# Kernel tuning notes

Measured on AMD Instinct MI355X. Metric: run time of the kernel, lower is better.

## Reference

```python
import jax, jax.numpy as jnp
import numpy as np

B, S, D, H = 2, 2048, 512, 8
HD = D // H
EPS = 1e-5


def _ln(x, g, b):
    mu = jnp.mean(x, axis=-1, keepdims=True)
    var = jnp.mean((x - mu) ** 2, axis=-1, keepdims=True)
    return (x - mu) * jax.lax.rsqrt(var + EPS) * g + b


def setup_inputs() -> dict:
    key = jax.random.key(0)
    ks = jax.random.split(key, 16)
    x = jax.random.normal(ks[0], (B, S, D), dtype=jnp.float32)
    adj = jax.random.randint(ks[1], (B, S, S), 0, 2, dtype=jnp.int32)
    adj = adj.at[:, jnp.arange(S), jnp.arange(S)].set(1)  # self-loops, avoid all-masked rows
    edge_attr = jax.random.normal(ks[2], (B, S, S), dtype=jnp.float32)
    sc = 1.0 / np.sqrt(D)
    p = lambda k, shp: jax.random.normal(k, shp, dtype=jnp.float32) * sc
    return {
        "x": x, "adj_matrix": adj, "edge_attr_matrix": edge_attr,
        "ln1_g": jnp.ones((D,)), "ln1_b": jnp.zeros((D,)),
        "ln2_g": jnp.ones((D,)), "ln2_b": jnp.zeros((D,)),
        "wq": p(ks[3], (D, D)), "bq": jnp.zeros((D,)),
        "wk": p(ks[4], (D, D)), "bk": jnp.zeros((D,)),
        "wv": p(ks[5], (D, D)), "bv": jnp.zeros((D,)),
        "wo": p(ks[6], (D, D)), "bo": jnp.zeros((D,)),
        "w1": p(ks[7], (D, 4 * D)), "b1": jnp.zeros((4 * D,)),
        "w2": p(ks[8], (4 * D, D)), "b2": jnp.zeros((D,)),
    }


def reference(x, adj_matrix, edge_attr_matrix, ln1_g, ln1_b, ln2_g, ln2_b,
              wq, bq, wk, bk, wv, bv, wo, bo, w1, b1, w2, b2):
    b, s, d = x.shape
    residual = x
    nx = _ln(x, ln1_g, ln1_b)
    q = (nx @ wq + bq).reshape(b, s, H, HD).transpose(0, 2, 1, 3)  # [B,H,S,HD]
    k = (nx @ wk + bk).reshape(b, s, H, HD).transpose(0, 2, 1, 3)
    v = (nx @ wv + bv).reshape(b, s, H, HD).transpose(0, 2, 1, 3)
    adjf = adj_matrix.astype(jnp.float32)
    # bias: -inf where no edge, else 0.1*edge_attr*adj (faithful to score_mod)
    bias = jnp.where(adj_matrix > 0, 0.1 * edge_attr_matrix * adjf, -jnp.inf)[:, None]  # [B,1,S,S]
    scores = jnp.einsum('bhqd,bhkd->bhqk', q, k) / np.sqrt(HD) + bias
    attn = jax.nn.softmax(scores, axis=-1)
    out = jnp.einsum('bhqk,bhkd->bhqd', attn, v)
    out = out.transpose(0, 2, 1, 3).reshape(b, s, d)
    x1 = residual + (out @ wo + bo)
    n2 = _ln(x1, ln2_g, ln2_b)
    mlp = jax.nn.gelu(n2 @ w1 + b1, approximate=False) @ w2 + b2
    return x1 + mlp
```

## Files before the change

kernel.cpp:

```cpp
#include <hip/hip_runtime.h>
#include <cstdint>
#include <cstddef>

typedef __bf16 bf16x8 __attribute__((ext_vector_type(8)));
typedef float f32x4 __attribute__((ext_vector_type(4)));
typedef const __attribute__((address_space(1))) void* gas_t;
typedef __attribute__((address_space(3))) void* las_t;

#define QSCALE 0.18033688011112042f
#define BSCALE 0.14426950408889634f

__device__ __forceinline__ unsigned short f2bf(float f) {
  union { float f; unsigned u; } v; v.f = f;
  unsigned r = v.u + 0x7FFFu + ((v.u >> 16) & 1u);
  return (unsigned short)(r >> 16);
}
__device__ __forceinline__ float bf2f(unsigned short h) {
  union { unsigned u; float f; } v; v.u = ((unsigned)h) << 16;
  return v.f;
}
__device__ __forceinline__ unsigned pack_bf16(float p0, float p1) {
  union { float f; unsigned u; } a, b; a.f = p0; b.f = p1;
  return __builtin_amdgcn_perm(b.u + 0x8000u, a.u + 0x8000u, 0x07060302u);
}
__device__ __forceinline__ void gll16(const void* g, void* l) {
  __builtin_amdgcn_global_load_lds((gas_t)g, (las_t)l, 16, 0, 0);
}

struct TPAll { const float* in[6]; unsigned short* out[6]; int R[6]; int C[6]; };
__global__ __launch_bounds__(256) void transpose_all(TPAll p) {
  const int z = blockIdx.z;
  int bxb = blockIdx.x, byb = blockIdx.y;
  if (z == 5) { int t = bxb; bxb = byb; byb = t; }
  const int R = p.R[z], C = p.C[z];
  const int bx = bxb * 32, by = byb * 32;
  if (bx >= C || by >= R) return;
  const float* in = p.in[z];
  unsigned short* out = p.out[z];
  __shared__ float tile[32][33];
  int tx = threadIdx.x & 31, tg = threadIdx.x >> 5;
  #pragma unroll
  for (int i = 0; i < 4; i++) {
    int r = tg * 4 + i;
    tile[r][tx] = in[(size_t)(by + r) * C + bx + tx];
  }
  __syncthreads();
  #pragma unroll
  for (int i = 0; i < 4; i++) {
    int r = tg * 4 + i;
    out[(size_t)(bx + r) * R + by + tx] = f2bf(tile[tx][r]);
  }
}

__global__ __launch_bounds__(256) void bias_pack(const int* __restrict__ adj,
                                                 const float* __restrict__ edge,
                                                 unsigned short* __restrict__ bp) {
  size_t i = ((size_t)blockIdx.x * 256 + threadIdx.x) * 4;
  int4 a = *(const int4*)(adj + i);
  float4 e = *(const float4*)(edge + i);
  ushort4 r;
  r.x = a.x > 0 ? f2bf(BSCALE * e.x * (float)a.x - 20.0f) : f2bf(-30000.0f);
  r.y = a.y > 0 ? f2bf(BSCALE * e.y * (float)a.y - 20.0f) : f2bf(-30000.0f);
  r.z = a.z > 0 ? f2bf(BSCALE * e.z * (float)a.z - 20.0f) : f2bf(-30000.0f);
  r.w = a.w > 0 ? f2bf(BSCALE * e.w * (float)a.w - 20.0f) : f2bf(-30000.0f);
  *(ushort4*)(bp + i) = r;
}

__global__ __launch_bounds__(256) void ln_kernel(const float* __restrict__ x,
                                                 const float* __restrict__ g,
                                                 const float* __restrict__ bt,
                                                 unsigned short* __restrict__ out) {
  int row = blockIdx.x, tid = threadIdx.x;
  float2 v = *(const float2*)(x + (size_t)row * 512 + tid * 2);
  float s = v.x + v.y, s2 = v.x * v.x + v.y * v.y;
  #pragma unroll
  for (int m = 1; m < 64; m <<= 1) { s += __shfl_xor(s, m, 64); s2 += __shfl_xor(s2, m, 64); }
  __shared__ float red[8];
  int w = tid >> 6;
  if ((tid & 63) == 0) { red[w * 2] = s; red[w * 2 + 1] = s2; }
  __syncthreads();
  float ts = red[0] + red[2] + red[4] + red[6];
  float ts2 = red[1] + red[3] + red[5] + red[7];
  float mu = ts * (1.0f / 512.0f);
  float rs = rsqrtf(ts2 * (1.0f / 512.0f) - mu * mu + 1e-5f);
  int c = tid * 2;
  ushort2 o;
  o.x = f2bf((v.x - mu) * rs * g[c] + bt[c]);
  o.y = f2bf((v.y - mu) * rs * g[c + 1] + bt[c + 1]);
  *(ushort2*)(out + (size_t)row * 512 + c) = o;
}

__global__ __launch_bounds__(256) void ln_fuse2(const float* __restrict__ x,
                                                const unsigned short* __restrict__ opp,
                                                const float* __restrict__ bo,
                                                const float* __restrict__ g,
                                                const float* __restrict__ bt,
                                                float* __restrict__ x1,
                                                unsigned short* __restrict__ n2) {
  const size_t MN = (size_t)4096 * 512;
  int row = blockIdx.x, tid = threadIdx.x;
  int c = tid * 2;
  size_t idx = (size_t)row * 512 + c;
  float2 xv = *(const float2*)(x + idx);
  ushort2 p0 = *(const ushort2*)(opp + idx);
  ushort2 p1 = *(const ushort2*)(opp + MN + idx);
  float2 v;
  v.x = xv.x + bo[c]     + bf2f(p0.x) + bf2f(p1.x);
  v.y = xv.y + bo[c + 1] + bf2f(p0.y) + bf2f(p1.y);
  float s = v.x + v.y, s2 = v.x * v.x + v.y * v.y;
  #pragma unroll
  for (int m = 1; m < 64; m <<= 1) { s += __shfl_xor(s, m, 64); s2 += __shfl_xor(s2, m, 64); }
  __shared__ float red[8];
  int w = tid >> 6;
  if ((tid & 63) == 0) { red[w * 2] = s; red[w * 2 + 1] = s2; }
  __syncthreads();
  float ts = red[0] + red[2] + red[4] + red[6];
  float ts2 = red[1] + red[3] + red[5] + red[7];
  float mu = ts * (1.0f / 512.0f);
  float rs = rsqrtf(ts2 * (1.0f / 512.0f) - mu * mu + 1e-5f);
  *(float2*)(x1 + idx) = v;
  ushort2 o;
  o.x = f2bf((v.x - mu) * rs * g[c] + bt[c]);
  o.y = f2bf((v.y - mu) * rs * g[c + 1] + bt[c + 1]);
  *(ushort2*)(n2 + idx) = o;
}

__global__ __launch_bounds__(256) void final_combine(const float* __restrict__ x1,
                                                     const float* __restrict__ b2,
                                                     const unsigned short* __restrict__ mp,
                                                     float* __restrict__ out) {
  const size_t MN = (size_t)4096 * 512;
  size_t i = ((size_t)blockIdx.x * 256 + threadIdx.x) * 4;
  float4 xv = *(const float4*)(x1 + i);
  float4 bv = *(const float4*)(b2 + (i & 511));
  float4 a;
  a.x = xv.x + bv.x; a.y = xv.y + bv.y; a.z = xv.z + bv.z; a.w = xv.w + bv.w;
  #pragma unroll
  for (int sp = 0; sp < 4; sp++) {
    ushort4 p = *(const ushort4*)(mp + sp * MN + i);
    a.x += bf2f(p.x); a.y += bf2f(p.y); a.z += bf2f(p.z); a.w += bf2f(p.w);
  }
  *(float4*)(out + i) = a;
}

struct EpiQKV {
  unsigned short *q, *k, *v;
  const float *bq, *bk, *bv;
  __device__ void operator()(int m, int n, float val) const {
    int b = m >> 11, s = m & 2047;
    int which = n >> 9, col = n & 511;
    int h = col >> 6, d = col & 63;
    int bh = b * 8 + h;
    if (which == 0)      q[((size_t)bh * 2048 + s) * 64 + d] = f2bf((val + bq[col]) * QSCALE);
    else if (which == 1) k[((size_t)bh * 2048 + s) * 64 + d] = f2bf(val + bk[col]);
    else                 v[((size_t)bh * 2048 + s) * 64 + d] = f2bf(val + bv[col]);
  }
};
struct EpiPart {
  unsigned short* dst; int ldn;
  __device__ void operator()(int m, int n, float val) const {
    dst[(size_t)blockIdx.z * 4096 * 512 + (size_t)m * ldn + n] = f2bf(val);
  }
};
struct EpiGelu {
  const float* b1; unsigned short* h;
  __device__ void operator()(int m, int n, float val) const {
    float t = val + b1[n];
    float gl = 0.5f * t * (1.0f + erff(t * 0.70710678118654752f));
    h[(size_t)m * 2048 + n] = f2bf(gl);
  }
};

template <typename Epi>
__global__ __launch_bounds__(256, 3) void gemm_bt(const unsigned short* __restrict__ A,
                                                  const unsigned short* __restrict__ Bt,
                                                  int lda, int ldb, int kchunk, Epi epi) {
  __shared__ unsigned short a_lds[128 * 64];
  __shared__ unsigned short b_lds[128 * 64];
  const int tid = threadIdx.x;
  const int lane = tid & 63;
  const int w = tid >> 6;
  const int l15 = lane & 15, quad = lane >> 4;
  const int wm = w >> 1, wn = w & 1;
  const int m0 = blockIdx.y * 128, n0 = blockIdx.x * 128;
  const int K0 = blockIdx.z * kchunk, K1 = K0 + kchunk;

  f32x4 acc[4][4] = {};

  for (int k0 = K0; k0 < K1; k0 += 64) {
    __syncthreads();
    #pragma unroll
    for (int i = 0; i < 4; i++) {
      int c = tid + i * 256;
      int g = c >> 6;
      int row = (g >> 1) * 16 + l15;
      int col = (g & 1) * 32 + quad * 8;
      gll16(A + (size_t)(m0 + row) * lda + k0 + col, a_lds + (size_t)(c & ~63) * 8);
      gll16(Bt + (size_t)(n0 + row) * ldb + k0 + col, b_lds + (size_t)(c & ~63) * 8);
    }
    __syncthreads();
    bf16x8 af[4][2], bfr[4][2];
    #pragma unroll
    for (int t = 0; t < 4; t++)
      #pragma unroll
      for (int ks = 0; ks < 2; ks++) {
        af[t][ks]  = *(const bf16x8*)(a_lds + (((size_t)(wm * 4 + t) * 2 + ks) * 64 + lane) * 8);
        bfr[t][ks] = *(const bf16x8*)(b_lds + (((size_t)(wn * 4 + t) * 2 + ks) * 64 + lane) * 8);
      }
    #pragma unroll
    for (int mt = 0; mt < 4; mt++)
      #pragma unroll
      for (int nt = 0; nt < 4; nt++) {
        acc[mt][nt] = __builtin_amdgcn_mfma_f32_16x16x32_bf16(af[mt][0], bfr[nt][0], acc[mt][nt], 0, 0, 0);
        acc[mt][nt] = __builtin_amdgcn_mfma_f32_16x16x32_bf16(af[mt][1], bfr[nt][1], acc[mt][nt], 0, 0, 0);
      }
  }
  #pragma unroll
  for (int mt = 0; mt < 4; mt++)
    #pragma unroll
    for (int nt = 0; nt < 4; nt++)
      #pragma unroll
      for (int r = 0; r < 4; r++)
        epi(m0 + wm * 64 + mt * 16 + quad * 4 + r, n0 + wn * 64 + nt * 16 + l15, acc[mt][nt][r]);
}

__global__ __launch_bounds__(256) void vt_kernel(const unsigned short* __restrict__ vb,
                                                 unsigned short* __restrict__ vbT) {
  __shared__ unsigned short tile[64][72];
  const int bh = blockIdx.y, s0 = blockIdx.x * 64;
  const int tid = threadIdx.x;
  const unsigned short* src = vb + ((size_t)bh * 2048 + s0) * 64;
  #pragma unroll
  for (int i = 0; i < 2; i++) {
    int r = (tid >> 3) + i * 32;
    int c8 = (tid & 7) * 8;
    *(uint4*)(&tile[r][c8]) = *(const uint4*)(src + (size_t)r * 64 + c8);
  }
  __syncthreads();
  unsigned short* dst = vbT + (size_t)bh * 64 * 2048 + s0;
  #pragma unroll
  for (int i = 0; i < 2; i++) {
    int d = (tid >> 3) + i * 32;
    int s8 = (tid & 7) * 8;
    ushort4 o0, o1;
    o0.x = tile[s8 + 0][d]; o0.y = tile[s8 + 1][d]; o0.z = tile[s8 + 2][d]; o0.w = tile[s8 + 3][d];
    o1.x = tile[s8 + 4][d]; o1.y = tile[s8 + 5][d]; o1.z = tile[s8 + 6][d]; o1.w = tile[s8 + 7][d];
    *(ushort4*)(dst + (size_t)d * 2048 + s8) = o0;
    *(ushort4*)(dst + (size_t)d * 2048 + s8 + 4) = o1;
  }
}

__global__ __launch_bounds__(256, 4) void attn_kernel(const unsigned short* __restrict__ Q,
                                                      const unsigned short* __restrict__ Kb,
                                                      const unsigned short* __restrict__ VT,
                                                      const unsigned short* __restrict__ biasp,
                                                      unsigned short* __restrict__ o_part,
                                                      float* __restrict__ l_part) {
  __shared__ unsigned short k_lds[2][64 * 64];
  __shared__ unsigned short v_lds[2][64 * 64];

  const int tid = threadIdx.x;
  const int lane = tid & 63, w = tid >> 6;
  const int l15 = lane & 15, quad = lane >> 4;
  const int bh = blockIdx.x, b = bh >> 3;
  const int q0 = blockIdx.y * 128 + w * 32;
  const int split = blockIdx.z;

  bf16x8 qf[2][2];
  const unsigned short* brow[2];
  #pragma unroll
  for (int g = 0; g < 2; g++) {
    const unsigned short* qrow = Q + ((size_t)bh * 2048 + q0 + g * 16 + l15) * 64;
    qf[g][0] = *(const bf16x8*)(qrow + quad * 8);
    qf[g][1] = *(const bf16x8*)(qrow + 32 + quad * 8);
    brow[g] = biasp + ((size_t)b * 2048 + q0 + g * 16 + l15) * 2048;
  }

  f32x4 o_acc[2][4] = {};
  float l_acc[2] = {0.0f, 0.0f};

  const unsigned short* kbase = Kb + (size_t)bh * 2048 * 64;
  const unsigned short* vbase = VT + (size_t)bh * 64 * 2048;

  const int srcA = ((lane & 16) << 1) | l15;
  const int srcB = srcA + 16;
  const bool hiTile = quad >= 2;

  const int kt0 = split * 8, kt1 = kt0 + 8;

  #pragma unroll
  for (int i = 0; i < 2; i++) {
    int c = tid + i * 256;
    int g = c >> 6;
    int rr = (g >> 1) * 16 + l15;
    int cc = (g & 1) * 32 + quad * 8;
    gll16(kbase + (size_t)(kt0 * 64 + rr) * 64 + cc, k_lds[0] + (size_t)(c & ~63) * 8);
    gll16(vbase + (size_t)rr * 2048 + kt0 * 64 + cc, v_lds[0] + (size_t)(c & ~63) * 8);
  }
  ushort4 blc[2][4];
  #pragma unroll
  for (int g = 0; g < 2; g++)
    #pragma unroll
    for (int mt = 0; mt < 4; mt++)
      blc[g][mt] = *(const ushort4*)(brow[g] + kt0 * 64 + mt * 16 + quad * 4);

  for (int kt = kt0; kt < kt1; kt++) {
    const int cur = (kt - kt0) & 1;
    const int kcol = kt * 64;
    __syncthreads();

    if (kt + 1 < kt1) {
      const int kcn = (kt + 1) * 64;
      #pragma unroll
      for (int i = 0; i < 2; i++) {
        int c = tid + i * 256;
        int g = c >> 6;
        int rr = (g >> 1) * 16 + l15;
        int cc = (g & 1) * 32 + quad * 8;
        gll16(kbase + (size_t)(kcn + rr) * 64 + cc, k_lds[1 - cur] + (size_t)(c & ~63) * 8);
        gll16(vbase + (size_t)rr * 2048 + kcn + cc, v_lds[1 - cur] + (size_t)(c & ~63) * 8);
      }
    }
    const int ktn64 = (kt + 1 < kt1) ? (kt + 1) * 64 : kcol;
    ushort4 bln[2][4];
    #pragma unroll
    for (int g = 0; g < 2; g++)
      #pragma unroll
      for (int mt = 0; mt < 4; mt++)
        bln[g][mt] = *(const ushort4*)(brow[g] + ktn64 + mt * 16 + quad * 4);

    #pragma unroll
    for (int H = 0; H < 2; H++) {
      bf16x8 kf[2][2];
      #pragma unroll
      for (int t = 0; t < 2; t++) {
        const int mtile = 2 * H + t;
        kf[t][0] = *(const bf16x8*)(k_lds[cur] + ((size_t)(mtile * 2 + 0) * 64 + lane) * 8);
        kf[t][1] = *(const bf16x8*)(k_lds[cur] + ((size_t)(mtile * 2 + 1) * 64 + lane) * 8);
      }
      unsigned pk[2][2][2];
      #pragma unroll
      for (int t = 0; t < 2; t++) {
        #pragma unroll
        for (int g = 0; g < 2; g++) {
          ushort4 bl = blc[g][2 * H + t];
          f32x4 cb;
          cb[0] = bf2f(bl.x); cb[1] = bf2f(bl.y); cb[2] = bf2f(bl.z); cb[3] = bf2f(bl.w);
          f32x4 s = __builtin_amdgcn_mfma_f32_16x16x32_bf16(kf[t][0], qf[g][0], cb, 0, 0, 0);
          s = __builtin_amdgcn_mfma_f32_16x16x32_bf16(kf[t][1], qf[g][1], s, 0, 0, 0);
          float p0 = exp2f(s[0]), p1 = exp2f(s[1]), p2 = exp2f(s[2]), p3 = exp2f(s[3]);
          l_acc[g] += (p0 + p1) + (p2 + p3);
          pk[t][g][0] = pack_bf16(p0, p1);
          pk[t][g][1] = pack_bf16(p2, p3);
        }
      }
      bf16x8 vf[4];
      #pragma unroll
      for (int dt = 0; dt < 4; dt++)
        vf[dt] = *(const bf16x8*)(v_lds[cur] + ((size_t)(dt * 2 + H) * 64 + lane) * 8);
      #pragma unroll
      for (int g = 0; g < 2; g++) {
        unsigned r0a = (unsigned)__shfl((int)pk[0][g][0], srcA);
        unsigned r0b = (unsigned)__shfl((int)pk[1][g][0], srcA);
        unsigned r1a = (unsigned)__shfl((int)pk[0][g][1], srcA);
        unsigned r1b = (unsigned)__shfl((int)pk[1][g][1], srcA);
        unsigned r2a = (unsigned)__shfl((int)pk[0][g][0], srcB);
        unsigned r2b = (unsigned)__shfl((int)pk[1][g][0], srcB);
        unsigned r3a = (unsigned)__shfl((int)pk[0][g][1], srcB);
        unsigned r3b = (unsigned)__shfl((int)pk[1][g][1], srcB);
        union { uint4 u; bf16x8 v; } fr;
        fr.u.x = hiTile ? r0b : r0a;
        fr.u.y = hiTile ? r1b : r1a;
        fr.u.z = hiTile ? r2b : r2a;
        fr.u.w = hiTile ? r3b : r3a;
        #pragma unroll
        for (int dt = 0; dt < 4; dt++)
          o_acc[g][dt] = __builtin_amdgcn_mfma_f32_16x16x32_bf16(fr.v, vf[dt], o_acc[g][dt], 0, 0, 0);
      }
    }

    #pragma unroll
    for (int g = 0; g < 2; g++)
      #pragma unroll
      for (int mt = 0; mt < 4; mt++)
        blc[g][mt] = bln[g][mt];
  }

  const size_t obase = ((size_t)split * 16 + bh) * 2048;
  #pragma unroll
  for (int g = 0; g < 2; g++) {
    float l = l_acc[g];
    l += __shfl_xor(l, 16, 64);
    l += __shfl_xor(l, 32, 64);
    if (quad == 0) l_part[obase + q0 + g * 16 + l15] = l;
    #pragma unroll
    for (int dt = 0; dt < 4; dt++)
      #pragma unroll
      for (int r = 0; r < 4; r++)
        o_part[(obase + q0 + g * 16 + quad * 4 + r) * 64 + dt * 16 + l15] =
            f2bf(o_acc[g][dt][r]);
  }
}

__global__ __launch_bounds__(256) void combine_kernel(const unsigned short* __restrict__ o_part,
                                                      const float* __restrict__ l_part,
                                                      unsigned short* __restrict__ ao) {
  const int row = blockIdx.x;
  const int b = row >> 11, s = row & 2047;
  const int col = threadIdx.x * 2;
  const int h = col >> 6, d = col & 63;
  const int bh = b * 8 + h;
  float ox = 0.0f, oy = 0.0f, l = 0.0f;
  #pragma unroll
  for (int sp = 0; sp < 4; sp++) {
    size_t base = (size_t)(sp * 16 + bh) * 2048 + s;
    ushort2 o = *(const ushort2*)(o_part + base * 64 + d);
    ox += bf2f(o.x); oy += bf2f(o.y);
    l += l_part[base];
  }
  float inv = 1.0f / l;
  ushort2 o;
  o.x = f2bf(ox * inv);
  o.y = f2bf(oy * inv);
  *(ushort2*)(ao + (size_t)row * 512 + col) = o;
}

extern "C" void kernel_launch(void* const* d_in, const int* in_sizes, int n_in,
                              void* d_out, int out_size, void* d_ws, size_t ws_size,
                              hipStream_t stream) {
  (void)in_sizes; (void)n_in; (void)out_size; (void)ws_size;
  const float* x    = (const float*)d_in[0];
  const int*   adj  = (const int*)d_in[1];
  const float* edge = (const float*)d_in[2];
  const float* ln1g = (const float*)d_in[3];
  const float* ln1b = (const float*)d_in[4];
  const float* ln2g = (const float*)d_in[5];
  const float* ln2b = (const float*)d_in[6];
  const float* wq = (const float*)d_in[7];  const float* bq = (const float*)d_in[8];
  const float* wk = (const float*)d_in[9];  const float* bk = (const float*)d_in[10];
  const float* wv = (const float*)d_in[11]; const float* bv = (const float*)d_in[12];
  const float* wo = (const float*)d_in[13]; const float* bo = (const float*)d_in[14];
  const float* w1 = (const float*)d_in[15]; const float* b1 = (const float*)d_in[16];
  const float* w2 = (const float*)d_in[17]; const float* b2 = (const float*)d_in[18];
  float* out = (float*)d_out;

  char* ws = (char*)d_ws;
  unsigned short* qkvT = (unsigned short*)ws; ws += (size_t)1536 * 512 * 2;
  unsigned short* woT  = (unsigned short*)ws; ws += (size_t)512 * 512 * 2;
  unsigned short* w1T  = (unsigned short*)ws; ws += (size_t)2048 * 512 * 2;
  unsigned short* w2T  = (unsigned short*)ws; ws += (size_t)512 * 2048 * 2;
  unsigned short* bp   = (unsigned short*)ws;
  unsigned short* opp  = (unsigned short*)ws; ws += (size_t)2 * 2048 * 2048 * 2;
  unsigned short* nx   = (unsigned short*)ws;
  unsigned short* n2   = (unsigned short*)ws; ws += (size_t)4096 * 512 * 2;
  unsigned short* qb   = (unsigned short*)ws;
  unsigned short* ao   = (unsigned short*)ws; ws += (size_t)4096 * 512 * 2;
  unsigned short* kb   = (unsigned short*)ws; ws += (size_t)4096 * 512 * 2;
  unsigned short* vb   = (unsigned short*)ws;
  float*          x1   = (float*)ws;          ws += (size_t)4096 * 512 * 2;
  unsigned short* vbT  = (unsigned short*)ws; ws += (size_t)4096 * 512 * 2;
  char* region1 = ws;
  unsigned short* opt  = (unsigned short*)region1;
  unsigned short* hb   = (unsigned short*)region1;
  float*          lpt  = (float*)(region1 + (size_t)4 * 16 * 2048 * 64 * 2);
  unsigned short* mp   = (unsigned short*)(region1 + (size_t)4 * 16 * 2048 * 64 * 2 + 524288);

  dim3 blk(256);
  TPAll tp;
  tp.in[0] = wq; tp.in[1] = wk; tp.in[2] = wv; tp.in[3] = wo; tp.in[4] = w1; tp.in[5] = w2;
  tp.out[0] = qkvT; tp.out[1] = qkvT + (size_t)512 * 512;
  tp.out[2] = qkvT + (size_t)2 * 512 * 512; tp.out[3] = woT; tp.out[4] = w1T; tp.out[5] = w2T;
  tp.R[0] = tp.R[1] = tp.R[2] = tp.R[3] = 512; tp.R[4] = 512; tp.R[5] = 2048;
  tp.C[0] = tp.C[1] = tp.C[2] = tp.C[3] = 512; tp.C[4] = 2048; tp.C[5] = 512;
  transpose_all<<<dim3(64, 16, 6), blk, 0, stream>>>(tp);
  bias_pack<<<8192, blk, 0, stream>>>(adj, edge, bp);
  ln_kernel<<<4096, blk, 0, stream>>>(x, ln1g, ln1b, nx);
  gemm_bt<<<dim3(12, 32, 1), blk, 0, stream>>>(nx, qkvT, 512, 512, 512,
                                               EpiQKV{qb, kb, vb, bq, bk, bv});
  vt_kernel<<<dim3(32, 16), blk, 0, stream>>>(vb, vbT);
  attn_kernel<<<dim3(16, 16, 4), blk, 0, stream>>>(qb, kb, vbT, bp, opt, lpt);
  combine_kernel<<<4096, blk, 0, stream>>>(opt, lpt, ao);
  gemm_bt<<<dim3(4, 32, 2), blk, 0, stream>>>(ao, woT, 512, 512, 256,
                                              EpiPart{opp, 512});
  ln_fuse2<<<4096, blk, 0, stream>>>(x, opp, bo, ln2g, ln2b, x1, n2);
  gemm_bt<<<dim3(16, 32, 1), blk, 0, stream>>>(n2, w1T, 512, 512, 512,
                                               EpiGelu{b1, hb});
  gemm_bt<<<dim3(4, 32, 4), blk, 0, stream>>>(hb, w2T, 2048, 2048, 512,
                                              EpiPart{mp, 512});
  final_combine<<<2048, blk, 0, stream>>>(x1, b2, mp, out);
}
```

Before: 318.2 us.

## Tile bias by key block, shrink GEMM N-tile, reorder attention grid

```diff
diff --git a/kernel.cpp b/kernel.cpp
--- a/kernel.cpp
+++ b/kernel.cpp
@@ -54,16 +54,26 @@
 
 __global__ __launch_bounds__(256) void bias_pack(const int* __restrict__ adj,
                                                  const float* __restrict__ edge,
-                                                 unsigned short* __restrict__ bp) {
-  size_t i = ((size_t)blockIdx.x * 256 + threadIdx.x) * 4;
-  int4 a = *(const int4*)(adj + i);
-  float4 e = *(const float4*)(edge + i);
-  ushort4 r;
-  r.x = a.x > 0 ? f2bf(BSCALE * e.x * (float)a.x - 20.0f) : f2bf(-30000.0f);
-  r.y = a.y > 0 ? f2bf(BSCALE * e.y * (float)a.y - 20.0f) : f2bf(-30000.0f);
-  r.z = a.z > 0 ? f2bf(BSCALE * e.z * (float)a.z - 20.0f) : f2bf(-30000.0f);
-  r.w = a.w > 0 ? f2bf(BSCALE * e.w * (float)a.w - 20.0f) : f2bf(-30000.0f);
-  *(ushort4*)(bp + i) = r;
+                                                 unsigned short* __restrict__ bpp) {
+  const int row = blockIdx.x;
+  const int b = row >> 11, q = row & 2047;
+  const int k0 = threadIdx.x * 8;
+  const size_t src = (size_t)row * 2048 + k0;
+  int4 a0 = *(const int4*)(adj + src);
+  int4 a1 = *(const int4*)(adj + src + 4);
+  float4 e0 = *(const float4*)(edge + src);
+  float4 e1 = *(const float4*)(edge + src + 4);
+  union { unsigned short u[8]; uint4 v; } o;
+  o.u[0] = a0.x > 0 ? f2bf(BSCALE * e0.x * (float)a0.x - 20.0f) : f2bf(-30000.0f);
+  o.u[1] = a0.y > 0 ? f2bf(BSCALE * e0.y * (float)a0.y - 20.0f) : f2bf(-30000.0f);
+  o.u[2] = a0.z > 0 ? f2bf(BSCALE * e0.z * (float)a0.z - 20.0f) : f2bf(-30000.0f);
+  o.u[3] = a0.w > 0 ? f2bf(BSCALE * e0.w * (float)a0.w - 20.0f) : f2bf(-30000.0f);
+  o.u[4] = a1.x > 0 ? f2bf(BSCALE * e1.x * (float)a1.x - 20.0f) : f2bf(-30000.0f);
+  o.u[5] = a1.y > 0 ? f2bf(BSCALE * e1.y * (float)a1.y - 20.0f) : f2bf(-30000.0f);
+  o.u[6] = a1.z > 0 ? f2bf(BSCALE * e1.z * (float)a1.z - 20.0f) : f2bf(-30000.0f);
+  o.u[7] = a1.w > 0 ? f2bf(BSCALE * e1.w * (float)a1.w - 20.0f) : f2bf(-30000.0f);
+  const int kt = k0 >> 6;
+  *(uint4*)(bpp + ((size_t)(b * 32 + kt) * 2048 + q) * 64 + (k0 & 63)) = o.v;
 }
 
 __global__ __launch_bounds__(256) void ln_kernel(const float* __restrict__ x,
@@ -172,20 +182,20 @@
 };
 
 template <typename Epi>
-__global__ __launch_bounds__(256, 3) void gemm_bt(const unsigned short* __restrict__ A,
+__global__ __launch_bounds__(256, 4) void gemm_bt(const unsigned short* __restrict__ A,
                                                   const unsigned short* __restrict__ Bt,
                                                   int lda, int ldb, int kchunk, Epi epi) {
   __shared__ unsigned short a_lds[128 * 64];
-  __shared__ unsigned short b_lds[128 * 64];
+  __shared__ unsigned short b_lds[64 * 64];
   const int tid = threadIdx.x;
   const int lane = tid & 63;
   const int w = tid >> 6;
   const int l15 = lane & 15, quad = lane >> 4;
-  const int wm = w >> 1, wn = w & 1;
-  const int m0 = blockIdx.y * 128, n0 = blockIdx.x * 128;
+  const int wm = w & 1, wn = w >> 1;
+  const int m0 = blockIdx.y * 128, n0 = blockIdx.x * 64;
   const int K0 = blockIdx.z * kchunk, K1 = K0 + kchunk;
 
-  f32x4 acc[4][4] = {};
+  f32x4 acc[4][2] = {};
 
   for (int k0 = K0; k0 < K1; k0 += 64) {
     __syncthreads();
@@ -196,21 +206,31 @@
       int row = (g >> 1) * 16 + l15;
       int col = (g & 1) * 32 + quad * 8;
       gll16(A + (size_t)(m0 + row) * lda + k0 + col, a_lds + (size_t)(c & ~63) * 8);
+    }
+    #pragma unroll
+    for (int i = 0; i < 2; i++) {
+      int c = tid + i * 256;
+      int g = c >> 6;
+      int row = (g >> 1) * 16 + l15;
+      int col = (g & 1) * 32 + quad * 8;
       gll16(Bt + (size_t)(n0 + row) * ldb + k0 + col, b_lds + (size_t)(c & ~63) * 8);
     }
     __syncthreads();
-    bf16x8 af[4][2], bfr[4][2];
+    bf16x8 af[4][2], bfr[2][2];
     #pragma unroll
     for (int t = 0; t < 4; t++)
       #pragma unroll
-      for (int ks = 0; ks < 2; ks++) {
-        af[t][ks]  = *(const bf16x8*)(a_lds + (((size_t)(wm * 4 + t) * 2 + ks) * 64 + lane) * 8);
-        bfr[t][ks] = *(const bf16x8*)(b_lds + (((size_t)(wn * 4 + t) * 2 + ks) * 64 + lane) * 8);
-      }
+      for (int ks = 0; ks < 2; ks++)
+        af[t][ks] = *(const bf16x8*)(a_lds + (((size_t)(wm * 4 + t) * 2 + ks) * 64 + lane) * 8);
+    #pragma unroll
+    for (int t = 0; t < 2; t++)
+      #pragma unroll
+      for (int ks = 0; ks < 2; ks++)
+        bfr[t][ks] = *(const bf16x8*)(b_lds + (((size_t)(wn * 2 + t) * 2 + ks) * 64 + lane) * 8);
     #pragma unroll
     for (int mt = 0; mt < 4; mt++)
       #pragma unroll
-      for (int nt = 0; nt < 4; nt++) {
+      for (int nt = 0; nt < 2; nt++) {
         acc[mt][nt] = __builtin_amdgcn_mfma_f32_16x16x32_bf16(af[mt][0], bfr[nt][0], acc[mt][nt], 0, 0, 0);
         acc[mt][nt] = __builtin_amdgcn_mfma_f32_16x16x32_bf16(af[mt][1], bfr[nt][1], acc[mt][nt], 0, 0, 0);
       }
@@ -218,10 +238,10 @@
   #pragma unroll
   for (int mt = 0; mt < 4; mt++)
     #pragma unroll
-    for (int nt = 0; nt < 4; nt++)
+    for (int nt = 0; nt < 2; nt++)
       #pragma unroll
       for (int r = 0; r < 4; r++)
-        epi(m0 + wm * 64 + mt * 16 + quad * 4 + r, n0 + wn * 64 + nt * 16 + l15, acc[mt][nt][r]);
+        epi(m0 + wm * 64 + mt * 16 + quad * 4 + r, n0 + wn * 32 + nt * 16 + l15, acc[mt][nt][r]);
 }
 
 __global__ __launch_bounds__(256) void vt_kernel(const unsigned short* __restrict__ vb,
@@ -253,7 +273,7 @@
 __global__ __launch_bounds__(256, 4) void attn_kernel(const unsigned short* __restrict__ Q,
                                                       const unsigned short* __restrict__ Kb,
                                                       const unsigned short* __restrict__ VT,
-                                                      const unsigned short* __restrict__ biasp,
+                                                      const unsigned short* __restrict__ bpp,
                                                       unsigned short* __restrict__ o_part,
                                                       float* __restrict__ l_part) {
   __shared__ unsigned short k_lds[2][64 * 64];
@@ -262,9 +282,10 @@
   const int tid = threadIdx.x;
   const int lane = tid & 63, w = tid >> 6;
   const int l15 = lane & 15, quad = lane >> 4;
-  const int bh = blockIdx.x, b = bh >> 3;
-  const int q0 = blockIdx.y * 128 + w * 32;
-  const int split = blockIdx.z;
+  const int qtile = blockIdx.x & 15, split = blockIdx.x >> 4;
+  const int b = blockIdx.z, h = blockIdx.y;
+  const int bh = b * 8 + h;
+  const int q0 = qtile * 128 + w * 32;
 
   bf16x8 qf[2][2];
   const unsigned short* brow[2];
@@ -273,7 +294,7 @@
     const unsigned short* qrow = Q + ((size_t)bh * 2048 + q0 + g * 16 + l15) * 64;
     qf[g][0] = *(const bf16x8*)(qrow + quad * 8);
     qf[g][1] = *(const bf16x8*)(qrow + 32 + quad * 8);
-    brow[g] = biasp + ((size_t)b * 2048 + q0 + g * 16 + l15) * 2048;
+    brow[g] = bpp + ((size_t)b * 32 * 2048 + q0 + g * 16 + l15) * 64;
   }
 
   f32x4 o_acc[2][4] = {};
@@ -302,11 +323,10 @@
   for (int g = 0; g < 2; g++)
     #pragma unroll
     for (int mt = 0; mt < 4; mt++)
-      blc[g][mt] = *(const ushort4*)(brow[g] + kt0 * 64 + mt * 16 + quad * 4);
+      blc[g][mt] = *(const ushort4*)(brow[g] + (size_t)kt0 * 131072 + mt * 16 + quad * 4);
 
   for (int kt = kt0; kt < kt1; kt++) {
     const int cur = (kt - kt0) & 1;
-    const int kcol = kt * 64;
     __syncthreads();
 
     if (kt + 1 < kt1) {
@@ -321,13 +341,13 @@
         gll16(vbase + (size_t)rr * 2048 + kcn + cc, v_lds[1 - cur] + (size_t)(c & ~63) * 8);
       }
     }
-    const int ktn64 = (kt + 1 < kt1) ? (kt + 1) * 64 : kcol;
+    const int ktn = (kt + 1 < kt1) ? kt + 1 : kt;
     ushort4 bln[2][4];
     #pragma unroll
     for (int g = 0; g < 2; g++)
       #pragma unroll
       for (int mt = 0; mt < 4; mt++)
-        bln[g][mt] = *(const ushort4*)(brow[g] + ktn64 + mt * 16 + quad * 4);
+        bln[g][mt] = *(const ushort4*)(brow[g] + (size_t)ktn * 131072 + mt * 16 + quad * 4);
 
     #pragma unroll
     for (int H = 0; H < 2; H++) {
@@ -473,19 +493,19 @@
   tp.R[0] = tp.R[1] = tp.R[2] = tp.R[3] = 512; tp.R[4] = 512; tp.R[5] = 2048;
   tp.C[0] = tp.C[1] = tp.C[2] = tp.C[3] = 512; tp.C[4] = 2048; tp.C[5] = 512;
   transpose_all<<<dim3(64, 16, 6), blk, 0, stream>>>(tp);
-  bias_pack<<<8192, blk, 0, stream>>>(adj, edge, bp);
+  bias_pack<<<4096, blk, 0, stream>>>(adj, edge, bp);
   ln_kernel<<<4096, blk, 0, stream>>>(x, ln1g, ln1b, nx);
-  gemm_bt<<<dim3(12, 32, 1), blk, 0, stream>>>(nx, qkvT, 512, 512, 512,
+  gemm_bt<<<dim3(24, 32, 1), blk, 0, stream>>>(nx, qkvT, 512, 512, 512,
                                                EpiQKV{qb, kb, vb, bq, bk, bv});
   vt_kernel<<<dim3(32, 16), blk, 0, stream>>>(vb, vbT);
-  attn_kernel<<<dim3(16, 16, 4), blk, 0, stream>>>(qb, kb, vbT, bp, opt, lpt);
+  attn_kernel<<<dim3(64, 8, 2), blk, 0, stream>>>(qb, kb, vbT, bp, opt, lpt);
   combine_kernel<<<4096, blk, 0, stream>>>(opt, lpt, ao);
-  gemm_bt<<<dim3(4, 32, 2), blk, 0, stream>>>(ao, woT, 512, 512, 256,
+  gemm_bt<<<dim3(8, 32, 2), blk, 0, stream>>>(ao, woT, 512, 512, 256,
                                               EpiPart{opp, 512});
   ln_fuse2<<<4096, blk, 0, stream>>>(x, opp, bo, ln2g, ln2b, x1, n2);
-  gemm_bt<<<dim3(16, 32, 1), blk, 0, stream>>>(n2, w1T, 512, 512, 512,
+  gemm_bt<<<dim3(32, 32, 1), blk, 0, stream>>>(n2, w1T, 512, 512, 512,
                                                EpiGelu{b1, hb});
-  gemm_bt<<<dim3(4, 32, 4), blk, 0, stream>>>(hb, w2T, 2048, 2048, 512,
+  gemm_bt<<<dim3(8, 32, 4), blk, 0, stream>>>(hb, w2T, 2048, 2048, 512,
                                               EpiPart{mp, 512});
   final_combine<<<2048, blk, 0, stream>>>(x1, b2, mp, out);
 }
```

After: 335.1 us. 5.3% more time.
